# Kernel optimization log

Hardware: AMD Instinct MI355X
Metric: run time of the kernel (lower is better)

The kernel has to match this reference:

```python
import jax, jax.numpy as jnp
import numpy as np

D_MODEL = 1024
N_HEADS = 16
N_GROUPS = 4
D_K = D_MODEL // N_HEADS
HEADS_PER_GROUP = N_HEADS // N_GROUPS


def rope(x):
    # x: [b, s, d]; rotate using half-split concat (NOT interleaved), matching source
    s, d = x.shape[1], x.shape[2]
    theta = 1.0 / (10000.0 ** (jnp.arange(d // 2, dtype=jnp.float32) / (d // 2)))
    ang = jnp.arange(s, dtype=jnp.float32)[:, None] * theta[None, :]  # [s, d/2]
    cos, sin = jnp.cos(ang), jnp.sin(ang)
    xe, xo = x[..., 0::2], x[..., 1::2]
    return jnp.concatenate([xe * cos - xo * sin, xe * sin + xo * cos], axis=-1)


def setup_inputs() -> dict:
    key = jax.random.key(0)
    k1, k2, k3, k4, k5 = jax.random.split(key, 5)
    b, s = 1, 2048
    scale = 0.02
    X = jax.random.normal(k1, (b, s, D_MODEL), dtype=jnp.float32)
    W_q = jax.random.normal(k2, (D_MODEL, D_MODEL), dtype=jnp.float32) * scale
    W_k = jax.random.normal(k3, (N_GROUPS * D_K, D_MODEL), dtype=jnp.float32) * scale
    W_v = jax.random.normal(k4, (N_GROUPS * D_K, D_MODEL), dtype=jnp.float32) * scale
    W_o = jax.random.normal(k5, (D_MODEL, D_MODEL), dtype=jnp.float32) * scale
    return {"X": X, "W_q": W_q, "W_k": W_k, "W_v": W_v, "W_o": W_o}


def reference(X, W_q, W_k, W_v, W_o):
    b, s, _ = X.shape
    Xr = rope(X)
    Q = (Xr @ W_q.T).reshape(b, s, N_HEADS, D_K).transpose(0, 2, 1, 3)
    K = (Xr @ W_k.T).reshape(b, s, N_GROUPS, D_K).transpose(0, 2, 1, 3)
    V = (Xr @ W_v.T).reshape(b, s, N_GROUPS, D_K).transpose(0, 2, 1, 3)
    Q = Q.reshape(b, N_GROUPS, HEADS_PER_GROUP, s, D_K)
    scores = jnp.einsum('bghsd,bgtd->bghst', Q, K) / jnp.sqrt(jnp.float32(D_K))
    mask = jnp.triu(jnp.ones((s, s), dtype=scores.dtype), k=1) * (-1e9)
    attn = jax.nn.softmax(scores + mask, axis=-1)
    out = jnp.einsum('bghst,bgtd->bghsd', attn, V)  # [b,g,h,s,dk]
    out = out.reshape(b, N_HEADS, s, D_K).transpose(0, 2, 1, 3).reshape(b, s, D_MODEL)
    return out @ W_o.T
```

## Files before the change

kernel.cpp:

```cpp
#include <hip/hip_runtime.h>
#include <hip/hip_bf16.h>

#define S_LEN   2048
#define D_MODEL 1024
#define N_HEADS 16
#define N_GROUPS 4
#define D_K     64
#define KV_DIM  (N_GROUPS * D_K)

typedef __hip_bfloat16 bf16;
typedef unsigned short u16;
typedef __attribute__((ext_vector_type(8))) short bfrag;
typedef __attribute__((ext_vector_type(4))) float ffrag;
typedef __attribute__((ext_vector_type(4))) unsigned int u32x4;

__device__ __forceinline__ float b2f(u16 u) {
    return __uint_as_float(((unsigned)u) << 16);
}
__device__ __forceinline__ u16 f2bu(float f) {
    bf16 h = __float2bfloat16(f);
    return __builtin_bit_cast(u16, h);
}
__device__ __forceinline__ unsigned cvt_pk_bf16(float lo, float hi) {
    unsigned r;
    asm("v_cvt_pk_bf16_f32 %0, %1, %2" : "=v"(r) : "v"(lo), "v"(hi));
    return r;
}
__device__ __forceinline__ float ex2(float x) {
#if __has_builtin(__builtin_amdgcn_exp2f)
    return __builtin_amdgcn_exp2f(x);
#else
    return __expf(x * 0.69314718f);
#endif
}

__global__ void probe5_kernel(const u16* __restrict__ p0, const u16* __restrict__ p1,
                              const u16* __restrict__ p2, const u16* __restrict__ p3,
                              const u16* __restrict__ p4, int* __restrict__ mode) {
    if (blockIdx.x != 0) return;
    const u16* ps[5] = {p0, p1, p2, p3, p4};
    int lane = threadIdx.x & 63;
    for (int t = 0; t < 5; t++) {
        int e0 = (ps[t][lane] >> 7) & 0xFF;
        int e1 = (ps[t][lane + 64] >> 7) & 0xFF;
        int c = ((e0 < 100 || e0 > 140) ? 1 : 0) + ((e1 < 100 || e1 > 140) ? 1 : 0);
        unsigned long long b1 = __ballot(c >= 1);
        unsigned long long b2 = __ballot(c >= 2);
        if (lane == 0) mode[t] = ((__popcll(b1) + __popcll(b2)) > 16) ? 1 : 0;
    }
}

__global__ __launch_bounds__(512)
void rope_kernel(const void* __restrict__ Xin, u16* __restrict__ Xr,
                 const int* __restrict__ mode) {
    int i = blockIdx.x;
    int j = threadIdx.x;
    int md = mode[0];
    float freq = powf(10000.0f, -(float)j * (1.0f / 512.0f));
    float ang  = (float)i * freq;
    float sv, cv;
    sincosf(ang, &sv, &cv);
    int base = i * D_MODEL;
    float xe, xo;
    if (md) {
        float2 xv = *(const float2*)&((const float*)Xin)[base + 2 * j];
        xe = xv.x; xo = xv.y;
    } else {
        ushort2 xv = *(const ushort2*)&((const u16*)Xin)[base + 2 * j];
        xe = b2f(xv.x); xo = b2f(xv.y);
    }
    Xr[base + j]       = f2bu(xe * cv - xo * sv);
    Xr[base + 512 + j] = f2bu(xe * sv + xo * cv);
}

__device__ __forceinline__ void stageB(u16* dst, const void* Bv, size_t off, int md) {
    if (md) {
        const float* Bf = (const float*)Bv;
        float4 b0 = *(const float4*)&Bf[off];
        float4 b1 = *(const float4*)&Bf[off + 4];
        u16 t[8] = {f2bu(b0.x), f2bu(b0.y), f2bu(b0.z), f2bu(b0.w),
                    f2bu(b1.x), f2bu(b1.y), f2bu(b1.z), f2bu(b1.w)};
        *(uint4*)dst = *(const uint4*)t;
    } else {
        *(uint4*)dst = *(const uint4*)&((const u16*)Bv)[off];
    }
}

__global__ __launch_bounds__(256)
void qkv_mfma(const u16* __restrict__ Xr, const void* __restrict__ Wq,
              const void* __restrict__ Wk, const void* __restrict__ Wv,
              u16* __restrict__ Qm, u16* __restrict__ Km, u16* __restrict__ Vm,
              const int* __restrict__ mode) {
    __shared__ u16 As[128][36];
    __shared__ u16 Bs[64][36];
    const int tid = threadIdx.x;
    const int w = tid >> 6, lane = tid & 63, quad = lane >> 4, lcol = lane & 15;
    const int m0 = blockIdx.y * 128;
    const int n0 = blockIdx.x * 64;

    const void* Bv; int nb, md;
    if (n0 < 1024)       { Bv = Wq; nb = n0;        md = mode[1]; }
    else if (n0 < 1280)  { Bv = Wk; nb = n0 - 1024; md = mode[2]; }
    else                 { Bv = Wv; nb = n0 - 1280; md = mode[3]; }

    ffrag acc[2][4];
    #pragma unroll
    for (int rf = 0; rf < 2; rf++)
        #pragma unroll
        for (int ct = 0; ct < 4; ct++) acc[rf][ct] = (ffrag)0.0f;

    const int arow = tid >> 2, akc = tid & 3;
    for (int k0 = 0; k0 < D_MODEL; k0 += 32) {
        *(uint4*)&As[arow][akc * 8] =
            *(const uint4*)&Xr[(size_t)(m0 + arow) * D_MODEL + k0 + akc * 8];
        *(uint4*)&As[arow + 64][akc * 8] =
            *(const uint4*)&Xr[(size_t)(m0 + arow + 64) * D_MODEL + k0 + akc * 8];
        stageB(&Bs[arow][akc * 8], Bv, (size_t)(nb + arow) * D_MODEL + k0 + akc * 8, md);
        __syncthreads();
        const bfrag a0 = *(const bfrag*)&As[w * 32 + lcol][quad * 8];
        const bfrag a1 = *(const bfrag*)&As[w * 32 + 16 + lcol][quad * 8];
        #pragma unroll
        for (int ct = 0; ct < 4; ct++) {
            const bfrag b = *(const bfrag*)&Bs[ct * 16 + lcol][quad * 8];
            acc[0][ct] = __builtin_amdgcn_mfma_f32_16x16x32_bf16(a0, b, acc[0][ct], 0, 0, 0);
            acc[1][ct] = __builtin_amdgcn_mfma_f32_16x16x32_bf16(a1, b, acc[1][ct], 0, 0, 0);
        }
        __syncthreads();
    }

    if (n0 < 1280) {
        u16* Cp; int ldc, nc;
        if (n0 < 1024) { Cp = Qm; ldc = 1024; nc = n0; }
        else           { Cp = Km; ldc = 256;  nc = n0 - 1024; }
        #pragma unroll
        for (int rf = 0; rf < 2; rf++)
            #pragma unroll
            for (int ct = 0; ct < 4; ct++)
                #pragma unroll
                for (int r = 0; r < 4; r++) {
                    int row = m0 + w * 32 + rf * 16 + quad * 4 + r;
                    Cp[(size_t)row * ldc + nc + ct * 16 + lcol] = f2bu(acc[rf][ct][r]);
                }
    } else {
        const int nc = n0 - 1280;
        #pragma unroll
        for (int rf = 0; rf < 2; rf++)
            #pragma unroll
            for (int ct = 0; ct < 4; ct++)
                #pragma unroll
                for (int r = 0; r < 4; r++) {
                    int row = m0 + w * 32 + rf * 16 + quad * 4 + r;
                    int col = nc + ct * 16 + lcol;
                    Vm[(size_t)col * S_LEN + row] = f2bu(acc[rf][ct][r]);
                }
    }
}

__global__ __launch_bounds__(256)
void oproj_mfma(const u16* __restrict__ A, const void* __restrict__ B,
                float* __restrict__ C, const int* __restrict__ mode) {
    __shared__ u16 As[128][36];
    __shared__ u16 Bs[64][36];
    const int tid = threadIdx.x;
    const int w = tid >> 6, lane = tid & 63, quad = lane >> 4, lcol = lane & 15;
    const int m0 = blockIdx.y * 128;
    const int n0 = blockIdx.x * 64;
    const int md = mode[4];

    ffrag acc[2][4];
    #pragma unroll
    for (int rf = 0; rf < 2; rf++)
        #pragma unroll
        for (int ct = 0; ct < 4; ct++) acc[rf][ct] = (ffrag)0.0f;

    const int arow = tid >> 2, akc = tid & 3;
    for (int k0 = 0; k0 < D_MODEL; k0 += 32) {
        *(uint4*)&As[arow][akc * 8] =
            *(const uint4*)&A[(size_t)(m0 + arow) * D_MODEL + k0 + akc * 8];
        *(uint4*)&As[arow + 64][akc * 8] =
            *(const uint4*)&A[(size_t)(m0 + arow + 64) * D_MODEL + k0 + akc * 8];
        stageB(&Bs[arow][akc * 8], B, (size_t)(n0 + arow) * D_MODEL + k0 + akc * 8, md);
        __syncthreads();
        const bfrag a0 = *(const bfrag*)&As[w * 32 + lcol][quad * 8];
        const bfrag a1 = *(const bfrag*)&As[w * 32 + 16 + lcol][quad * 8];
        #pragma unroll
        for (int ct = 0; ct < 4; ct++) {
            const bfrag b = *(const bfrag*)&Bs[ct * 16 + lcol][quad * 8];
            acc[0][ct] = __builtin_amdgcn_mfma_f32_16x16x32_bf16(a0, b, acc[0][ct], 0, 0, 0);
            acc[1][ct] = __builtin_amdgcn_mfma_f32_16x16x32_bf16(a1, b, acc[1][ct], 0, 0, 0);
        }
        __syncthreads();
    }

    #pragma unroll
    for (int rf = 0; rf < 2; rf++)
        #pragma unroll
        for (int ct = 0; ct < 4; ct++)
            #pragma unroll
            for (int r = 0; r < 4; r++) {
                int row = m0 + w * 32 + rf * 16 + quad * 4 + r;
                C[(size_t)row * D_MODEL + n0 + ct * 16 + lcol] = acc[rf][ct][r];
            }
}

template<int CS, int SF>
__global__ __launch_bounds__(256)
void attn_part(const u16* __restrict__ Q, const u16* __restrict__ K,
               const u16* __restrict__ Vt, float* __restrict__ OpF,
               u16* __restrict__ OpH, float2* __restrict__ ml2) {
    const int bid = blockIdx.x;
    const int cidx = bid >> 4;
    const int h = bid & 15;
    const int g = h >> 2;

    int i, c;
    if (CS == 3) {
        if (cidx < 8)       { i = cidx;                  c = 0; }
        else if (cidx < 24) { i = 8 + ((cidx - 8) >> 1); c = (cidx - 8) & 1; }
        else if (cidx < 48) { int q = (cidx - 24) / 3;   i = 16 + q; c = (cidx - 24) - 3 * q; }
        else                { i = 24 + ((cidx - 48) >> 2); c = (cidx - 48) & 3; }
    } else {
        if (cidx < 16) { i = cidx; c = 0; }
        else           { i = 16 + ((cidx - 16) >> 1); c = (cidx - 16) & 1; }
    }
    const int i0 = i * 64;
    const int tile0 = c << CS;
    const int tlast = min(i, ((c + 1) << CS) - 1);
    const int nt = tlast - tile0 + 1;

    const int tid  = threadIdx.x;
    const int w    = tid >> 6;
    const int lane = tid & 63;
    const int quad = lane >> 4;
    const int lcol = lane & 15;

    __shared__ u16 Ks[64][72];
    __shared__ u16 Vts[64][72];

    const int qi = i0 + w * 16 + lcol;
    const bfrag qb0 = *(const bfrag*)&Q[(size_t)qi * D_MODEL + h * 64 + quad * 8];
    const bfrag qb1 = *(const bfrag*)&Q[(size_t)qi * D_MODEL + h * 64 + 32 + quad * 8];

    ffrag oacc[4];
    #pragma unroll
    for (int ct = 0; ct < 4; ct++) oacc[ct] = (ffrag)0.0f;
    float m_run = -1e30f, l_run = 0.0f;

    const int key0 = tid & 63, dc0 = tid >> 6;
    const int vd0 = tid >> 3, vch = tid & 7;
    const int vpos0 = 32 * (vch >> 2) + 16 * (vch & 1) + 4 * ((vch >> 1) & 1);
    const u16* vbase0 = &Vt[(size_t)(g * 64 + vd0) * S_LEN];
    const u16* vbase1 = &Vt[(size_t)(g * 64 + vd0 + 32) * S_LEN];

    int jp = tile0 * 64;
    uint4 kpre0 = *(const uint4*)&K[(size_t)(jp + key0) * KV_DIM + g * 64 + dc0 * 8];
    uint4 kpre1 = *(const uint4*)&K[(size_t)(jp + key0) * KV_DIM + g * 64 + (dc0 + 4) * 8];
    uint4 vpre0 = *(const uint4*)&vbase0[jp + vch * 8];
    uint4 vpre1 = *(const uint4*)&vbase1[jp + vch * 8];

    const float CF = 0.18033688f;

    for (int tt = 0; tt < nt; tt++) {
        const int j0 = (tile0 + tt) * 64;

        *(uint4*)&Ks[key0][dc0 * 8]       = kpre0;
        *(uint4*)&Ks[key0][(dc0 + 4) * 8] = kpre1;
        *(uint2*)&Vts[vd0][vpos0]           = make_uint2(vpre0.x, vpre0.y);
        *(uint2*)&Vts[vd0][vpos0 + 8]       = make_uint2(vpre0.z, vpre0.w);
        *(uint2*)&Vts[vd0 + 32][vpos0]      = make_uint2(vpre1.x, vpre1.y);
        *(uint2*)&Vts[vd0 + 32][vpos0 + 8]  = make_uint2(vpre1.z, vpre1.w);
        __syncthreads();

        if (tt + 1 < nt) {
            const int j0n = (tile0 + tt + 1) * 64;
            kpre0 = *(const uint4*)&K[(size_t)(j0n + key0) * KV_DIM + g * 64 + dc0 * 8];
            kpre1 = *(const uint4*)&K[(size_t)(j0n + key0) * KV_DIM + g * 64 + (dc0 + 4) * 8];
            vpre0 = *(const uint4*)&vbase0[j0n + vch * 8];
            vpre1 = *(const uint4*)&vbase1[j0n + vch * 8];
        }

        ffrag sacc[4];
        #pragma unroll
        for (int ct = 0; ct < 4; ct++) sacc[ct] = (ffrag)0.0f;
        #pragma unroll
        for (int ct = 0; ct < 4; ct++) {
            const bfrag kb0 = *(const bfrag*)&Ks[ct * 16 + lcol][quad * 8];
            sacc[ct] = __builtin_amdgcn_mfma_f32_16x16x32_bf16(kb0, qb0, sacc[ct], 0, 0, 0);
            const bfrag kb1 = *(const bfrag*)&Ks[ct * 16 + lcol][32 + quad * 8];
            sacc[ct] = __builtin_amdgcn_mfma_f32_16x16x32_bf16(kb1, qb1, sacc[ct], 0, 0, 0);
        }

        float sv[4][4];
        if (tile0 + tt == i) {
            #pragma unroll
            for (int ct = 0; ct < 4; ct++)
                #pragma unroll
                for (int r = 0; r < 4; r++) {
                    int kj = j0 + ct * 16 + quad * 4 + r;
                    sv[ct][r] = (kj <= qi) ? sacc[ct][r] : -1e30f;
                }
        } else {
            #pragma unroll
            for (int ct = 0; ct < 4; ct++)
                #pragma unroll
                for (int r = 0; r < 4; r++) sv[ct][r] = sacc[ct][r];
        }

        float mx = sv[0][0];
        #pragma unroll
        for (int ct = 0; ct < 4; ct++)
            #pragma unroll
            for (int r = 0; r < 4; r++) mx = fmaxf(mx, sv[ct][r]);
        mx = fmaxf(mx, __shfl_xor(mx, 16, 64));
        mx = fmaxf(mx, __shfl_xor(mx, 32, 64));

        if (!__all(mx <= m_run + 44.0f)) {
            float mnew = fmaxf(m_run, mx);
            float al = ex2((m_run - mnew) * CF);
            m_run = mnew;
            l_run *= al;
            #pragma unroll
            for (int r = 0; r < 4; r++) {
                float ar = __shfl(al, quad * 4 + r, 64);
                #pragma unroll
                for (int ct = 0; ct < 4; ct++) oacc[ct][r] *= ar;
            }
        }

        const float mc = m_run * CF;
        float rs = 0.0f;
        #pragma unroll
        for (int ct = 0; ct < 4; ct++)
            #pragma unroll
            for (int r = 0; r < 4; r++) {
                float p = ex2(sv[ct][r] * CF - mc);
                sv[ct][r] = p;
                rs += p;
            }
        rs += __shfl_xor(rs, 16, 64);
        rs += __shfl_xor(rs, 32, 64);
        l_run += rs;

        u32x4 pw0, pw1;
        pw0[0] = cvt_pk_bf16(sv[0][0], sv[0][1]);
        pw0[1] = cvt_pk_bf16(sv[0][2], sv[0][3]);
        pw0[2] = cvt_pk_bf16(sv[1][0], sv[1][1]);
        pw0[3] = cvt_pk_bf16(sv[1][2], sv[1][3]);
        pw1[0] = cvt_pk_bf16(sv[2][0], sv[2][1]);
        pw1[1] = cvt_pk_bf16(sv[2][2], sv[2][3]);
        pw1[2] = cvt_pk_bf16(sv[3][0], sv[3][1]);
        pw1[3] = cvt_pk_bf16(sv[3][2], sv[3][3]);
        const bfrag pa0 = __builtin_bit_cast(bfrag, pw0);
        const bfrag pa1 = __builtin_bit_cast(bfrag, pw1);

        #pragma unroll
        for (int ct = 0; ct < 4; ct++) {
            const bfrag vb0 = *(const bfrag*)&Vts[ct * 16 + lcol][quad * 8];
            oacc[ct] = __builtin_amdgcn_mfma_f32_16x16x32_bf16(pa0, vb0, oacc[ct], 0, 0, 0);
            const bfrag vb1 = *(const bfrag*)&Vts[ct * 16 + lcol][32 + quad * 8];
            oacc[ct] = __builtin_amdgcn_mfma_f32_16x16x32_bf16(pa1, vb1, oacc[ct], 0, 0, 0);
        }
        __syncthreads();
    }

    #pragma unroll
    for (int ct = 0; ct < 4; ct++)
        #pragma unroll
        for (int r = 0; r < 4; r++) {
            int row = w * 16 + quad * 4 + r;
            size_t off = (size_t)bid * 4096 + row * 64 + ct * 16 + lcol;
            if (SF) OpF[off] = oacc[ct][r];
            else    OpH[off] = f2bu(oacc[ct][r]);
        }
    if (quad == 0)
        ml2[(size_t)bid * 64 + w * 16 + lcol] = make_float2(m_run * 0.125f, l_run);
}

template<int CS, int SF>
__global__ __launch_bounds__(256)
void attn_combine(const float* __restrict__ OpF, const u16* __restrict__ OpH,
                  const float2* __restrict__ ml2, u16* __restrict__ Om) {
    const int row = blockIdx.x;
    const int i = row >> 6;
    const int r = row & 63;
    const int t = threadIdx.x;
    const int h = t >> 4;
    const int d = (t & 15) * 4;
    const int nc = (i >> CS) + 1;
    int pfx;
    if (CS == 3)
        pfx = (i < 8) ? i : (i < 16) ? 8 + 2 * (i - 8)
            : (i < 24) ? 24 + 3 * (i - 16) : 48 + 4 * (i - 24);
    else
        pfx = (i < 16) ? i : 16 + 2 * (i - 16);

    float M = -1e30f;
    for (int c = 0; c < nc; c++) {
        float2 m = ml2[(size_t)((pfx + c) * 16 + h) * 64 + r];
        M = fmaxf(M, m.x);
    }
    float L = 0.0f;
    float acc[4] = {0.0f, 0.0f, 0.0f, 0.0f};
    for (int c = 0; c < nc; c++) {
        float2 m = ml2[(size_t)((pfx + c) * 16 + h) * 64 + r];
        float wgt = __expf(m.x - M);
        L += m.y * wgt;
        size_t off = (size_t)((pfx + c) * 16 + h) * 4096 + r * 64 + d;
        if (SF) {
            float4 v = *(const float4*)&OpF[off];
            acc[0] += v.x * wgt; acc[1] += v.y * wgt;
            acc[2] += v.z * wgt; acc[3] += v.w * wgt;
        } else {
            ushort4 v = *(const ushort4*)&OpH[off];
            acc[0] += b2f(v.x) * wgt; acc[1] += b2f(v.y) * wgt;
            acc[2] += b2f(v.z) * wgt; acc[3] += b2f(v.w) * wgt;
        }
    }
    float inv = 1.0f / L;
    #pragma unroll
    for (int k = 0; k < 4; k++)
        Om[(size_t)row * D_MODEL + h * 64 + d + k] = f2bu(acc[k] * inv);
}

extern "C" void kernel_launch(void* const* d_in, const int* in_sizes, int n_in,
                              void* d_out, int out_size, void* d_ws, size_t ws_size,
                              hipStream_t stream) {
    const void* X  = d_in[0];
    const void* Wq = d_in[1];
    const void* Wk = d_in[2];
    const void* Wv = d_in[3];
    const void* Wo = d_in[4];
    float* out = (float*)d_out;

    u16* XrB = (u16*)d_out;

    int* mode = (int*)d_ws;
    u16* Qm = (u16*)((char*)d_ws + 64);
    u16* Km = Qm + (size_t)S_LEN * D_MODEL;
    u16* Vm = Km + (size_t)S_LEN * KV_DIM;
    u16* Om = Vm + (size_t)S_LEN * KV_DIM;

    probe5_kernel<<<1, 64, 0, stream>>>(
        (const u16*)X, (const u16*)Wq, (const u16*)Wk, (const u16*)Wv,
        (const u16*)Wo, mode);

    rope_kernel<<<S_LEN, 512, 0, stream>>>(X, XrB, mode + 0);

    qkv_mfma<<<dim3((D_MODEL + 2 * KV_DIM) / 64, S_LEN / 128), 256, 0, stream>>>(
        XrB, Wq, Wk, Wv, Qm, Km, Vm, mode);

    const size_t needA = 10485824ULL + 20971520ULL + 655360ULL;
    if (ws_size >= needA) {
        float*  OpF = (float*)((char*)d_ws + 10485824);
        float2* ml2 = (float2*)((char*)d_ws + 10485824 + 20971520);
        attn_part<3, 1><<<80 * 16, 256, 0, stream>>>(Qm, Km, Vm, OpF, nullptr, ml2);
        attn_combine<3, 1><<<S_LEN, 256, 0, stream>>>(OpF, nullptr, ml2, Om);
    } else {
        u16*    OpH = (u16*)d_out;
        float2* ml2 = (float2*)((char*)d_out + (size_t)768 * 4096 * 2);
        attn_part<4, 0><<<48 * 16, 256, 0, stream>>>(Qm, Km, Vm, nullptr, OpH, ml2);
        attn_combine<4, 0><<<S_LEN, 256, 0, stream>>>(nullptr, OpH, ml2, Om);
    }

    oproj_mfma<<<dim3(D_MODEL / 64, S_LEN / 128), 256, 0, stream>>>(Om, Wo, out, mode);
}
```

Before: 167.8 us.

## Pre-convert weights to bf16 and use direct-to-LDS GEMM for projections

Adds a weight conversion kernel that writes all projection weights as bf16 into the workspace, then runs new GEMM kernels that stage tiles with global_load_lds into swizzled LDS for the QKV and output projections. The separate probe kernel is folded into each consumer, RoPE uses exp2 instead of powf, and s_setprio raises wave priority around the attention MFMA blocks. This targets per-tile fp32-to-bf16 conversion in the GEMMs and launch overhead, at the cost of an extra conversion pass and more workspace, with the new path taken only when the workspace is large enough.

```diff
diff --git a/kernel.cpp b/kernel.cpp
--- a/kernel.cpp
+++ b/kernel.cpp
@@ -32,6 +32,22 @@
 #else
     return __expf(x * 0.69314718f);
 #endif
+}
+
+typedef __attribute__((address_space(3))) u16 lds_u16;
+typedef __attribute__((address_space(1))) const u16 glb_u16;
+__device__ __forceinline__ void gld_lds16(const u16* g, u16* l) {
+    __builtin_amdgcn_global_load_lds((glb_u16*)g, (lds_u16*)l, 16, 0, 0);
+}
+
+__device__ __forceinline__ int probe_f32(const u16* p) {
+    int lane = threadIdx.x & 63;
+    int e0 = (p[lane] >> 7) & 0xFF;
+    int e1 = (p[lane + 64] >> 7) & 0xFF;
+    int c = ((e0 < 100 || e0 > 140) ? 1 : 0) + ((e1 < 100 || e1 > 140) ? 1 : 0);
+    unsigned long long b1 = __ballot(c >= 1);
+    unsigned long long b2 = __ballot(c >= 2);
+    return ((__popcll(b1) + __popcll(b2)) > 16) ? 1 : 0;
 }
 
 __global__ void probe5_kernel(const u16* __restrict__ p0, const u16* __restrict__ p1,
@@ -51,12 +67,11 @@
 }
 
 __global__ __launch_bounds__(512)
-void rope_kernel(const void* __restrict__ Xin, u16* __restrict__ Xr,
-                 const int* __restrict__ mode) {
+void rope_kernel(const void* __restrict__ Xin, u16* __restrict__ Xr) {
+    int md = probe_f32((const u16*)Xin);
     int i = blockIdx.x;
     int j = threadIdx.x;
-    int md = mode[0];
-    float freq = powf(10000.0f, -(float)j * (1.0f / 512.0f));
+    float freq = ex2(-(float)j * 0.025952563241307518f);
     float ang  = (float)i * freq;
     float sv, cv;
     sincosf(ang, &sv, &cv);
@@ -73,6 +88,132 @@
     Xr[base + 512 + j] = f2bu(xe * sv + xo * cv);
 }
 
+__global__ __launch_bounds__(256)
+void wconv_kernel(const void* __restrict__ Wq, const void* __restrict__ Wk,
+                  const void* __restrict__ Wv, const void* __restrict__ Wo,
+                  u16* __restrict__ WB, u16* __restrict__ WoB) {
+    int bid = blockIdx.x;
+    const void* src; u16* dst; int gbase;
+    if (bid < 512)      { src = Wq; dst = WB;                      gbase = bid; }
+    else if (bid < 640) { src = Wk; dst = WB + 1024 * 1024;        gbase = bid - 512; }
+    else if (bid < 768) { src = Wv; dst = WB + 1280 * 1024;        gbase = bid - 640; }
+    else                { src = Wo; dst = WoB;                     gbase = bid - 768; }
+    int md = probe_f32((const u16*)src);
+    size_t g = (size_t)gbase * 256 + threadIdx.x;
+    if (md) {
+        const float* f = (const float*)src + g * 8;
+        float4 v0 = *(const float4*)f;
+        float4 v1 = *(const float4*)(f + 4);
+        u16 t[8] = {f2bu(v0.x), f2bu(v0.y), f2bu(v0.z), f2bu(v0.w),
+                    f2bu(v1.x), f2bu(v1.y), f2bu(v1.z), f2bu(v1.w)};
+        *(uint4*)(dst + g * 8) = *(const uint4*)t;
+    } else {
+        *(uint4*)(dst + g * 8) = *(const uint4*)((const u16*)src + g * 8);
+    }
+}
+
+template<int MODE>
+__global__ __launch_bounds__(256)
+void gemm_fast(const u16* __restrict__ A, const u16* __restrict__ WBm,
+               u16* __restrict__ Qm, u16* __restrict__ Km, u16* __restrict__ Vm,
+               float* __restrict__ Cf) {
+    __shared__ u16 As[8192];
+    __shared__ u16 Bs[4096];
+    const int tid = threadIdx.x;
+    const int w = tid >> 6, lane = tid & 63, quad = lane >> 4, lcol = lane & 15;
+    const int m0 = blockIdx.y * 128;
+    const int n0 = blockIdx.x * 64;
+
+    const int arl   = lane >> 3;
+    const int colsw = ((lane & 7) ^ arl) * 8;
+
+    const u16* ap[4]; const u16* bp[2];
+    u16* asd[4]; u16* bsd[2];
+    #pragma unroll
+    for (int c = 0; c < 4; c++) {
+        ap[c]  = A + (size_t)(m0 + (c * 4 + w) * 8 + arl) * 1024 + colsw;
+        asd[c] = As + (c * 4 + w) * 512;
+    }
+    #pragma unroll
+    for (int c = 0; c < 2; c++) {
+        bp[c]  = WBm + (size_t)(n0 + (c * 4 + w) * 8 + arl) * 1024 + colsw;
+        bsd[c] = Bs + (c * 4 + w) * 512;
+    }
+
+    const int abase = (w * 32 + lcol) * 64;
+    const int koff0 = (quad * 8) ^ ((lcol & 7) * 8);
+    const int koff1 = koff0 ^ 32;
+
+    ffrag acc[2][4];
+    #pragma unroll
+    for (int rf = 0; rf < 2; rf++)
+        #pragma unroll
+        for (int ct = 0; ct < 4; ct++) acc[rf][ct] = (ffrag)0.0f;
+
+    for (int k0 = 0; k0 < D_MODEL; k0 += 64) {
+        #pragma unroll
+        for (int c = 0; c < 4; c++) gld_lds16(ap[c] + k0, asd[c]);
+        #pragma unroll
+        for (int c = 0; c < 2; c++) gld_lds16(bp[c] + k0, bsd[c]);
+        __syncthreads();
+
+        const bfrag a00 = *(const bfrag*)&As[abase + koff0];
+        const bfrag a10 = *(const bfrag*)&As[abase + 1024 + koff0];
+        const bfrag a01 = *(const bfrag*)&As[abase + koff1];
+        const bfrag a11 = *(const bfrag*)&As[abase + 1024 + koff1];
+        #pragma unroll
+        for (int ct = 0; ct < 4; ct++) {
+            const int bb = (ct * 16 + lcol) * 64;
+            const bfrag b0 = *(const bfrag*)&Bs[bb + koff0];
+            acc[0][ct] = __builtin_amdgcn_mfma_f32_16x16x32_bf16(a00, b0, acc[0][ct], 0, 0, 0);
+            acc[1][ct] = __builtin_amdgcn_mfma_f32_16x16x32_bf16(a10, b0, acc[1][ct], 0, 0, 0);
+            const bfrag b1 = *(const bfrag*)&Bs[bb + koff1];
+            acc[0][ct] = __builtin_amdgcn_mfma_f32_16x16x32_bf16(a01, b1, acc[0][ct], 0, 0, 0);
+            acc[1][ct] = __builtin_amdgcn_mfma_f32_16x16x32_bf16(a11, b1, acc[1][ct], 0, 0, 0);
+        }
+        __syncthreads();
+    }
+
+    if (MODE == 0) {
+        if (n0 < 1280) {
+            u16* Cp; int ldc, nc;
+            if (n0 < 1024) { Cp = Qm; ldc = 1024; nc = n0; }
+            else           { Cp = Km; ldc = 256;  nc = n0 - 1024; }
+            #pragma unroll
+            for (int rf = 0; rf < 2; rf++)
+                #pragma unroll
+                for (int ct = 0; ct < 4; ct++)
+                    #pragma unroll
+                    for (int r = 0; r < 4; r++) {
+                        int row = m0 + w * 32 + rf * 16 + quad * 4 + r;
+                        Cp[(size_t)row * ldc + nc + ct * 16 + lcol] = f2bu(acc[rf][ct][r]);
+                    }
+        } else {
+            const int nc = n0 - 1280;
+            #pragma unroll
+            for (int rf = 0; rf < 2; rf++)
+                #pragma unroll
+                for (int ct = 0; ct < 4; ct++)
+                    #pragma unroll
+                    for (int r = 0; r < 4; r++) {
+                        int row = m0 + w * 32 + rf * 16 + quad * 4 + r;
+                        int col = nc + ct * 16 + lcol;
+                        Vm[(size_t)col * S_LEN + row] = f2bu(acc[rf][ct][r]);
+                    }
+        }
+    } else {
+        #pragma unroll
+        for (int rf = 0; rf < 2; rf++)
+            #pragma unroll
+            for (int ct = 0; ct < 4; ct++)
+                #pragma unroll
+                for (int r = 0; r < 4; r++) {
+                    int row = m0 + w * 32 + rf * 16 + quad * 4 + r;
+                    Cf[(size_t)row * D_MODEL + n0 + ct * 16 + lcol] = acc[rf][ct][r];
+                }
+    }
+}
+
 __device__ __forceinline__ void stageB(u16* dst, const void* Bv, size_t off, int md) {
     if (md) {
         const float* Bf = (const float*)Bv;
@@ -282,6 +423,7 @@
         ffrag sacc[4];
         #pragma unroll
         for (int ct = 0; ct < 4; ct++) sacc[ct] = (ffrag)0.0f;
+        __builtin_amdgcn_s_setprio(1);
         #pragma unroll
         for (int ct = 0; ct < 4; ct++) {
             const bfrag kb0 = *(const bfrag*)&Ks[ct * 16 + lcol][quad * 8];
@@ -289,6 +431,7 @@
             const bfrag kb1 = *(const bfrag*)&Ks[ct * 16 + lcol][32 + quad * 8];
             sacc[ct] = __builtin_amdgcn_mfma_f32_16x16x32_bf16(kb1, qb1, sacc[ct], 0, 0, 0);
         }
+        __builtin_amdgcn_s_setprio(0);
 
         float sv[4][4];
         if (tile0 + tt == i) {
@@ -353,6 +496,7 @@
         const bfrag pa0 = __builtin_bit_cast(bfrag, pw0);
         const bfrag pa1 = __builtin_bit_cast(bfrag, pw1);
 
+        __builtin_amdgcn_s_setprio(1);
         #pragma unroll
         for (int ct = 0; ct < 4; ct++) {
             const bfrag vb0 = *(const bfrag*)&Vts[ct * 16 + lcol][quad * 8];
@@ -360,6 +504,7 @@
             const bfrag vb1 = *(const bfrag*)&Vts[ct * 16 + lcol][32 + quad * 8];
             oacc[ct] = __builtin_amdgcn_mfma_f32_16x16x32_bf16(pa1, vb1, oacc[ct], 0, 0, 0);
         }
+        __builtin_amdgcn_s_setprio(0);
         __syncthreads();
     }
 
@@ -440,27 +585,39 @@
     u16* Vm = Km + (size_t)S_LEN * KV_DIM;
     u16* Om = Vm + (size_t)S_LEN * KV_DIM;
 
-    probe5_kernel<<<1, 64, 0, stream>>>(
-        (const u16*)X, (const u16*)Wq, (const u16*)Wk, (const u16*)Wv,
-        (const u16*)Wo, mode);
-
-    rope_kernel<<<S_LEN, 512, 0, stream>>>(X, XrB, mode + 0);
-
-    qkv_mfma<<<dim3((D_MODEL + 2 * KV_DIM) / 64, S_LEN / 128), 256, 0, stream>>>(
-        XrB, Wq, Wk, Wv, Qm, Km, Vm, mode);
-
-    const size_t needA = 10485824ULL + 20971520ULL + 655360ULL;
-    if (ws_size >= needA) {
+    const size_t needA    = 10485824ULL + 20971520ULL + 655360ULL;
+    const size_t needFull = needA + 3145728ULL + 2097152ULL;
+
+    rope_kernel<<<S_LEN, 512, 0, stream>>>(X, XrB);
+
+    if (ws_size >= needFull) {
         float*  OpF = (float*)((char*)d_ws + 10485824);
         float2* ml2 = (float2*)((char*)d_ws + 10485824 + 20971520);
+        u16*    WB  = (u16*)((char*)d_ws + needA);
+        u16*    WoB = WB + (size_t)1536 * 1024;
+
+        wconv_kernel<<<1280, 256, 0, stream>>>(Wq, Wk, Wv, Wo, WB, WoB);
+        gemm_fast<0><<<dim3(24, 16), 256, 0, stream>>>(XrB, WB, Qm, Km, Vm, nullptr);
         attn_part<3, 1><<<80 * 16, 256, 0, stream>>>(Qm, Km, Vm, OpF, nullptr, ml2);
         attn_combine<3, 1><<<S_LEN, 256, 0, stream>>>(OpF, nullptr, ml2, Om);
+        gemm_fast<1><<<dim3(16, 16), 256, 0, stream>>>(Om, WoB, nullptr, nullptr, nullptr, out);
     } else {
-        u16*    OpH = (u16*)d_out;
-        float2* ml2 = (float2*)((char*)d_out + (size_t)768 * 4096 * 2);
-        attn_part<4, 0><<<48 * 16, 256, 0, stream>>>(Qm, Km, Vm, nullptr, OpH, ml2);
-        attn_combine<4, 0><<<S_LEN, 256, 0, stream>>>(nullptr, OpH, ml2, Om);
-    }
-
-    oproj_mfma<<<dim3(D_MODEL / 64, S_LEN / 128), 256, 0, stream>>>(Om, Wo, out, mode);
-}
+        probe5_kernel<<<1, 64, 0, stream>>>(
+            (const u16*)X, (const u16*)Wq, (const u16*)Wk, (const u16*)Wv,
+            (const u16*)Wo, mode);
+        qkv_mfma<<<dim3((D_MODEL + 2 * KV_DIM) / 64, S_LEN / 128), 256, 0, stream>>>(
+            XrB, Wq, Wk, Wv, Qm, Km, Vm, mode);
+        if (ws_size >= needA) {
+            float*  OpF = (float*)((char*)d_ws + 10485824);
+            float2* ml2 = (float2*)((char*)d_ws + 10485824 + 20971520);
+            attn_part<3, 1><<<80 * 16, 256, 0, stream>>>(Qm, Km, Vm, OpF, nullptr, ml2);
+            attn_combine<3, 1><<<S_LEN, 256, 0, stream>>>(OpF, nullptr, ml2, Om);
+        } else {
+            u16*    OpH = (u16*)d_out;
+            float2* ml2 = (float2*)((char*)d_out + (size_t)768 * 4096 * 2);
+            attn_part<4, 0><<<48 * 16, 256, 0, stream>>>(Qm, Km, Vm, nullptr, OpH, ml2);
+            attn_combine<4, 0><<<S_LEN, 256, 0, stream>>>(nullptr, OpH, ml2, Om);
+        }
+        oproj_mfma<<<dim3(D_MODEL / 64, S_LEN / 128), 256, 0, stream>>>(Om, Wo, out, mode);
+    }
+}
```

Result: faster. 144.6 us (-13.8%).
